# Kernel tuning notes

Measured on AMD Instinct MI355X. Metric: run time of the kernel, lower is better.

## Reference

```python
import jax, jax.numpy as jnp
import numpy as np

IM_SIZE = 32
SCALE = float(IM_SIZE ** 2)  # sqrt(im_size**4)


def setup_inputs() -> dict:
    key = jax.random.key(0)
    kq, kk, kv = jax.random.split(key, 3)
    shape = (2, 8, 64, IM_SIZE, IM_SIZE, 16)  # b n p x y d
    return {
        "query": jax.random.normal(kq, shape, dtype=jnp.float32),
        "key": jax.random.normal(kk, shape, dtype=jnp.float32),
        "value": jax.random.normal(kv, shape, dtype=jnp.float32),
    }


def reference(query, key, value):
    # scores: [b, n, p, q], contraction over the flattened (x, y, d) token field
    scores = jnp.einsum('bnpxyd,bnqxyd->bnpq', query, key) / SCALE
    attention_weights = jax.nn.softmax(scores, axis=-1)
    # dropout p=0.0 (eval mode) -> identity
    out = jnp.einsum('bnpq,bnqxyd->bnpxyd', attention_weights, value)
    out = jnp.transpose(out, (0, 2, 3, 4, 5, 1))  # -> [b, p, x, y, d, n]
    return (out, attention_weights)
```

## Files before the change

### kernel.cpp

```cpp
#include <hip/hip_runtime.h>
#include <hip/hip_bf16.h>

typedef __attribute__((ext_vector_type(8))) short short8;
typedef __attribute__((ext_vector_type(4))) float f32x4;

#define P64 64
#define FDIM 16384
#define OUT0 16777216

__device__ __forceinline__ unsigned short f2bf(float x) {
    unsigned int u = __float_as_uint(x);
    u += 0x7FFFu + ((u >> 16) & 1u);
    return (unsigned short)(u >> 16);
}

__device__ __forceinline__ short8 pack8(float4 v0, float4 v1) {
    short8 r;
    r[0] = (short)f2bf(v0.x); r[1] = (short)f2bf(v0.y);
    r[2] = (short)f2bf(v0.z); r[3] = (short)f2bf(v0.w);
    r[4] = (short)f2bf(v1.x); r[5] = (short)f2bf(v1.y);
    r[6] = (short)f2bf(v1.z); r[7] = (short)f2bf(v1.w);
    return r;
}

__global__ __launch_bounds__(256) void qk_kernel(
        const float* __restrict__ Q, const float* __restrict__ K,
        float* __restrict__ partials) {
    __shared__ float red[4][64 * 65];
    const int bn    = blockIdx.y;
    const int slice = blockIdx.x;
    const int wave  = threadIdx.x >> 6;
    const int lane  = threadIdx.x & 63;
    const int lrow  = lane & 15;
    const int lg    = lane >> 4;
    const int kbase0 = slice * 256 + wave * 64;

    const float* Qb = Q + (size_t)bn * P64 * FDIM;
    const float* Kb = K + (size_t)bn * P64 * FDIM;

    f32x4 acc[4][4];
#pragma unroll
    for (int i = 0; i < 4; i++)
#pragma unroll
        for (int j = 0; j < 4; j++) acc[i][j] = (f32x4){0.f, 0.f, 0.f, 0.f};

#pragma unroll
    for (int ks = 0; ks < 64; ks += 32) {
        const int kb = kbase0 + ks + lg * 8;
        short8 a[4], b[4];
#pragma unroll
        for (int pt = 0; pt < 4; pt++) {
            const float* src = Qb + (size_t)(pt * 16 + lrow) * FDIM + kb;
            a[pt] = pack8(*(const float4*)src, *(const float4*)(src + 4));
        }
#pragma unroll
        for (int qt = 0; qt < 4; qt++) {
            const float* src = Kb + (size_t)(qt * 16 + lrow) * FDIM + kb;
            b[qt] = pack8(*(const float4*)src, *(const float4*)(src + 4));
        }
#pragma unroll
        for (int pt = 0; pt < 4; pt++)
#pragma unroll
            for (int qt = 0; qt < 4; qt++)
                acc[pt][qt] = __builtin_amdgcn_mfma_f32_16x16x32_bf16(
                    a[pt], b[qt], acc[pt][qt], 0, 0, 0);
    }

#pragma unroll
    for (int pt = 0; pt < 4; pt++)
#pragma unroll
        for (int qt = 0; qt < 4; qt++)
#pragma unroll
            for (int r = 0; r < 4; r++) {
                const int p = pt * 16 + lg * 4 + r;
                const int q = qt * 16 + lrow;
                red[wave][p * 65 + q] = acc[pt][qt][r];
            }
    __syncthreads();

    float* dst = partials + ((size_t)bn * 64 + slice) * 4096;
#pragma unroll
    for (int e = threadIdx.x; e < 4096; e += 256) {
        const int p = e >> 6, q = e & 63;
        const int o = p * 65 + q;
        dst[e] = red[0][o] + red[1][o] + red[2][o] + red[3][o];
    }
}

__global__ __launch_bounds__(256) void softmax_kernel(
        const float* __restrict__ partials, float* __restrict__ attn_out) {
    const int wave = threadIdx.x >> 6;
    const int lane = threadIdx.x & 63;
    const int row  = blockIdx.x * 4 + wave;
    const int bn = row >> 6;
    const int p  = row & 63;

    const float* src = partials + (size_t)bn * 64 * 4096 + p * 64 + lane;
    float s = 0.f;
#pragma unroll 8
    for (int sl = 0; sl < 64; sl++) s += src[(size_t)sl * 4096];
    s *= (1.0f / 1024.0f);

    float m = s;
#pragma unroll
    for (int off = 32; off; off >>= 1) m = fmaxf(m, __shfl_xor(m, off, 64));
    const float e = __expf(s - m);
    float sum = e;
#pragma unroll
    for (int off = 32; off; off >>= 1) sum += __shfl_xor(sum, off, 64);
    attn_out[(size_t)row * 64 + lane] = e / sum;
}

__global__ __launch_bounds__(256) void pv_kernel(
        const float* __restrict__ V, const float* __restrict__ attn,
        float* __restrict__ out) {
    const int b  = blockIdx.y;
    const int fc = blockIdx.x * 16;
    const int wave = threadIdx.x >> 6;
    const int lane = threadIdx.x & 63;
    const int pstrip = wave * 16;
    const int lrow = lane & 15;
    const int lg   = lane >> 4;

    f32x4 acc[8];
#pragma unroll
    for (int n = 0; n < 8; n++) acc[n] = (f32x4){0.f, 0.f, 0.f, 0.f};

#pragma unroll
    for (int n = 0; n < 8; n++) {
        const float* An = attn + (size_t)(b * 8 + n) * 64 * 64;
        const float* Vn = V + (size_t)(b * 8 + n) * P64 * FDIM;

#pragma unroll
        for (int kk = 0; kk < 2; kk++) {
            const float* as = An + (size_t)(pstrip + lrow) * 64 + kk * 32 + lg * 8;
            const short8 a = pack8(*(const float4*)as, *(const float4*)(as + 4));
            const float* vs = Vn + (size_t)(kk * 32 + lg * 8) * FDIM + fc + lrow;
            short8 bf;
#pragma unroll
            for (int j = 0; j < 8; j++) bf[j] = (short)f2bf(vs[(size_t)j * FDIM]);
            acc[n] = __builtin_amdgcn_mfma_f32_16x16x32_bf16(a, bf, acc[n], 0, 0, 0);
        }
    }

#pragma unroll
    for (int r = 0; r < 4; r++) {
        const int p = pstrip + lg * 4 + r;
        float4 w0, w1;
        w0.x = acc[0][r]; w0.y = acc[1][r]; w0.z = acc[2][r]; w0.w = acc[3][r];
        w1.x = acc[4][r]; w1.y = acc[5][r]; w1.z = acc[6][r]; w1.w = acc[7][r];
        float* dst = out + ((size_t)(b * 64 + p) * FDIM + fc + lrow) * 8;
        *(float4*)dst       = w0;
        *(float4*)(dst + 4) = w1;
    }
}

extern "C" void kernel_launch(void* const* d_in, const int* in_sizes, int n_in,
                              void* d_out, int out_size, void* d_ws, size_t ws_size,
                              hipStream_t stream) {
    const float* Q = (const float*)d_in[0];
    const float* K = (const float*)d_in[1];
    const float* V = (const float*)d_in[2];
    float* out  = (float*)d_out;
    float* attn = out + OUT0;
    float* partials = (float*)d_ws;

    qk_kernel<<<dim3(64, 16), 256, 0, stream>>>(Q, K, partials);
    softmax_kernel<<<256, 256, 0, stream>>>(partials, attn);
    pv_kernel<<<dim3(1024, 2), 256, 0, stream>>>(V, attn, out);
}
```

Before: 272.5 us.

## Store bf16 per-wave QK partials and stage V tiles in LDS with double-buffering

The QK kernel drops its LDS cross-wave reduction and writes per-wave partial score tiles directly in bf16, so the softmax kernel now reduces 256 slices per row using a block per row. The PV kernel is restructured to load 64-wide V tiles into LDS via global_load_lds with double buffering across heads, so each V element is fetched once per block and coalesced. The aim is to cut strided global V reads and partial-buffer traffic. In exchange, partials are rounded to bf16 before summation, which adds precision loss, and the partials buffer gets larger.

After: 240.4 us. 1.13x faster.

```diff
diff --git a/kernel.cpp b/kernel.cpp
--- a/kernel.cpp
+++ b/kernel.cpp
@@ -4,16 +4,18 @@
 typedef __attribute__((ext_vector_type(8))) short short8;
 typedef __attribute__((ext_vector_type(4))) float f32x4;
 
-#define P64 64
 #define FDIM 16384
 #define OUT0 16777216
+#define NSL  256
 
 __device__ __forceinline__ unsigned short f2bf(float x) {
     unsigned int u = __float_as_uint(x);
     u += 0x7FFFu + ((u >> 16) & 1u);
     return (unsigned short)(u >> 16);
 }
-
+__device__ __forceinline__ float bf2f(unsigned short b) {
+    return __uint_as_float(((unsigned int)b) << 16);
+}
 __device__ __forceinline__ short8 pack8(float4 v0, float4 v1) {
     short8 r;
     r[0] = (short)f2bf(v0.x); r[1] = (short)f2bf(v0.y);
@@ -23,20 +25,18 @@
     return r;
 }
 
-__global__ __launch_bounds__(256) void qk_kernel(
+__global__ __launch_bounds__(256, 4) void qk_kernel(
         const float* __restrict__ Q, const float* __restrict__ K,
-        float* __restrict__ partials) {
-    __shared__ float red[4][64 * 65];
-    const int bn    = blockIdx.y;
-    const int slice = blockIdx.x;
-    const int wave  = threadIdx.x >> 6;
-    const int lane  = threadIdx.x & 63;
-    const int lrow  = lane & 15;
-    const int lg    = lane >> 4;
-    const int kbase0 = slice * 256 + wave * 64;
-
-    const float* Qb = Q + (size_t)bn * P64 * FDIM;
-    const float* Kb = K + (size_t)bn * P64 * FDIM;
+        unsigned short* __restrict__ partials) {
+    const int bn   = blockIdx.y;
+    const int wave = threadIdx.x >> 6;
+    const int lane = threadIdx.x & 63;
+    const int sl   = blockIdx.x * 4 + wave;
+    const int lrow = lane & 15;
+    const int lg   = lane >> 4;
+
+    const float* Qb = Q + (size_t)bn * 64 * FDIM;
+    const float* Kb = K + (size_t)bn * 64 * FDIM;
 
     f32x4 acc[4][4];
 #pragma unroll
@@ -46,7 +46,7 @@
 
 #pragma unroll
     for (int ks = 0; ks < 64; ks += 32) {
-        const int kb = kbase0 + ks + lg * 8;
+        const int kb = sl * 64 + ks + lg * 8;
         short8 a[4], b[4];
 #pragma unroll
         for (int pt = 0; pt < 4; pt++) {
@@ -74,85 +74,143 @@
             for (int r = 0; r < 4; r++) {
                 const int p = pt * 16 + lg * 4 + r;
                 const int q = qt * 16 + lrow;
-                red[wave][p * 65 + q] = acc[pt][qt][r];
+                partials[((size_t)(bn * 64 + p) * NSL + sl) * 64 + q] =
+                    f2bf(acc[pt][qt][r]);
             }
-    __syncthreads();
-
-    float* dst = partials + ((size_t)bn * 64 + slice) * 4096;
-#pragma unroll
-    for (int e = threadIdx.x; e < 4096; e += 256) {
-        const int p = e >> 6, q = e & 63;
-        const int o = p * 65 + q;
-        dst[e] = red[0][o] + red[1][o] + red[2][o] + red[3][o];
-    }
 }
 
 __global__ __launch_bounds__(256) void softmax_kernel(
-        const float* __restrict__ partials, float* __restrict__ attn_out) {
+        const unsigned short* __restrict__ partials, float* __restrict__ attn_out) {
+    __shared__ float red[4][64];
+    const int row  = blockIdx.x;
     const int wave = threadIdx.x >> 6;
     const int lane = threadIdx.x & 63;
-    const int row  = blockIdx.x * 4 + wave;
-    const int bn = row >> 6;
-    const int p  = row & 63;
-
-    const float* src = partials + (size_t)bn * 64 * 4096 + p * 64 + lane;
-    float s = 0.f;
-#pragma unroll 8
-    for (int sl = 0; sl < 64; sl++) s += src[(size_t)sl * 4096];
-    s *= (1.0f / 1024.0f);
-
-    float m = s;
-#pragma unroll
-    for (int off = 32; off; off >>= 1) m = fmaxf(m, __shfl_xor(m, off, 64));
-    const float e = __expf(s - m);
-    float sum = e;
-#pragma unroll
-    for (int off = 32; off; off >>= 1) sum += __shfl_xor(sum, off, 64);
-    attn_out[(size_t)row * 64 + lane] = e / sum;
-}
-
-__global__ __launch_bounds__(256) void pv_kernel(
+    const int gp   = lane >> 3;
+    const int o    = lane & 7;
+    const int g    = wave * 8 + gp;
+
+    const unsigned short* src = partials + (size_t)row * NSL * 64;
+    float s[8] = {0.f, 0.f, 0.f, 0.f, 0.f, 0.f, 0.f, 0.f};
+#pragma unroll
+    for (int i = 0; i < 8; i++) {
+        const int slc = g + 32 * i;
+        const short8 v = *(const short8*)(src + (size_t)slc * 64 + o * 8);
+#pragma unroll
+        for (int j = 0; j < 8; j++) s[j] += bf2f((unsigned short)v[j]);
+    }
+#pragma unroll
+    for (int off = 8; off <= 32; off <<= 1)
+#pragma unroll
+        for (int j = 0; j < 8; j++) s[j] += __shfl_xor(s[j], off, 64);
+    if (lane < 8)
+#pragma unroll
+        for (int j = 0; j < 8; j++) red[wave][lane * 8 + j] = s[j];
+    __syncthreads();
+
+    if (wave == 0) {
+        float t = red[0][lane] + red[1][lane] + red[2][lane] + red[3][lane];
+        t *= (1.0f / 1024.0f);
+        float m = t;
+#pragma unroll
+        for (int off = 32; off; off >>= 1) m = fmaxf(m, __shfl_xor(m, off, 64));
+        const float e = __expf(t - m);
+        float sum = e;
+#pragma unroll
+        for (int off = 32; off; off >>= 1) sum += __shfl_xor(sum, off, 64);
+        attn_out[(size_t)row * 64 + lane] = e / sum;
+    }
+}
+
+__global__ __launch_bounds__(512, 4) void pv_kernel(
         const float* __restrict__ V, const float* __restrict__ attn,
         float* __restrict__ out) {
-    const int b  = blockIdx.y;
-    const int fc = blockIdx.x * 16;
-    const int wave = threadIdx.x >> 6;
+    __shared__ float vt[2][64 * 64];
+    const int b    = blockIdx.y;
+    const int fc   = blockIdx.x * 64;
+    const int w    = threadIdx.x >> 6;
     const int lane = threadIdx.x & 63;
-    const int pstrip = wave * 16;
     const int lrow = lane & 15;
     const int lg   = lane >> 4;
-
-    f32x4 acc[8];
-#pragma unroll
-    for (int n = 0; n < 8; n++) acc[n] = (f32x4){0.f, 0.f, 0.f, 0.f};
-
+    const int pstrip = (w >> 1) * 16;
+    const int fstrip = (w & 1) * 32;
+
+    f32x4 acc[8][2];
+#pragma unroll
+    for (int n = 0; n < 8; n++)
+#pragma unroll
+        for (int ft = 0; ft < 2; ft++) acc[n][ft] = (f32x4){0.f, 0.f, 0.f, 0.f};
+
+#define STAGE(BI, N)                                                          \
+    {                                                                         \
+        const float* Vn_ = V + (size_t)(b * 8 + (N)) * 64 * FDIM;             \
+        _Pragma("unroll")                                                     \
+        for (int c = 0; c < 2; c++) {                                         \
+            const int row_ = w * 8 + c * 4 + lg;                              \
+            const float* src_ = Vn_ + (size_t)row_ * FDIM + fc + lrow * 4;    \
+            __builtin_amdgcn_global_load_lds(                                 \
+                (const __attribute__((address_space(1))) void*)src_,          \
+                (__attribute__((address_space(3))) void*)&vt[BI][row_ * 64 + lrow * 4], \
+                16, 0, 0);                                                    \
+        }                                                                     \
+    }
+
+    STAGE(0, 0);
 #pragma unroll
     for (int n = 0; n < 8; n++) {
-        const float* An = attn + (size_t)(b * 8 + n) * 64 * 64;
-        const float* Vn = V + (size_t)(b * 8 + n) * P64 * FDIM;
-
-#pragma unroll
-        for (int kk = 0; kk < 2; kk++) {
-            const float* as = An + (size_t)(pstrip + lrow) * 64 + kk * 32 + lg * 8;
-            const short8 a = pack8(*(const float4*)as, *(const float4*)(as + 4));
-            const float* vs = Vn + (size_t)(kk * 32 + lg * 8) * FDIM + fc + lrow;
-            short8 bf;
-#pragma unroll
-            for (int j = 0; j < 8; j++) bf[j] = (short)f2bf(vs[(size_t)j * FDIM]);
-            acc[n] = __builtin_amdgcn_mfma_f32_16x16x32_bf16(a, bf, acc[n], 0, 0, 0);
-        }
-    }
-
-#pragma unroll
-    for (int r = 0; r < 4; r++) {
-        const int p = pstrip + lg * 4 + r;
-        float4 w0, w1;
-        w0.x = acc[0][r]; w0.y = acc[1][r]; w0.z = acc[2][r]; w0.w = acc[3][r];
-        w1.x = acc[4][r]; w1.y = acc[5][r]; w1.z = acc[6][r]; w1.w = acc[7][r];
-        float* dst = out + ((size_t)(b * 64 + p) * FDIM + fc + lrow) * 8;
-        *(float4*)dst       = w0;
-        *(float4*)(dst + 4) = w1;
-    }
+        const int cur = n & 1;
+        const float* Ap = attn + (size_t)(b * 8 + n) * 4096 +
+                          (size_t)(pstrip + lrow) * 64 + lg * 8;
+        const float4 a00 = *(const float4*)(Ap);
+        const float4 a01 = *(const float4*)(Ap + 4);
+        const float4 a10 = *(const float4*)(Ap + 32);
+        const float4 a11 = *(const float4*)(Ap + 36);
+
+        if (n < 7) {
+            STAGE(cur ^ 1, n + 1);
+            asm volatile("s_waitcnt vmcnt(2)" ::: "memory");
+        } else {
+            asm volatile("s_waitcnt vmcnt(0)" ::: "memory");
+        }
+        __builtin_amdgcn_s_barrier();
+        __builtin_amdgcn_sched_barrier(0);
+
+        const short8 a0 = pack8(a00, a01);
+        const short8 a1 = pack8(a10, a11);
+
+#pragma unroll
+        for (int ft = 0; ft < 2; ft++) {
+#pragma unroll
+            for (int kk = 0; kk < 2; kk++) {
+                short8 bf;
+#pragma unroll
+                for (int j = 0; j < 8; j++) {
+                    const float vv = vt[cur][(kk * 32 + lg * 8 + j) * 64 +
+                                             fstrip + ft * 16 + lrow];
+                    bf[j] = (short)f2bf(vv);
+                }
+                acc[n][ft] = __builtin_amdgcn_mfma_f32_16x16x32_bf16(
+                    kk ? a1 : a0, bf, acc[n][ft], 0, 0, 0);
+            }
+        }
+        __builtin_amdgcn_s_barrier();
+    }
+
+#pragma unroll
+    for (int ft = 0; ft < 2; ft++)
+#pragma unroll
+        for (int r = 0; r < 4; r++) {
+            const int p = pstrip + lg * 4 + r;
+            const int f = fc + fstrip + ft * 16 + lrow;
+            float4 w0, w1;
+            w0.x = acc[0][ft][r]; w0.y = acc[1][ft][r];
+            w0.z = acc[2][ft][r]; w0.w = acc[3][ft][r];
+            w1.x = acc[4][ft][r]; w1.y = acc[5][ft][r];
+            w1.z = acc[6][ft][r]; w1.w = acc[7][ft][r];
+            float* dst = out + ((size_t)(b * 64 + p) * FDIM + f) * 8;
+            *(float4*)dst       = w0;
+            *(float4*)(dst + 4) = w1;
+        }
+#undef STAGE
 }
 
 extern "C" void kernel_launch(void* const* d_in, const int* in_sizes, int n_in,
@@ -163,9 +221,9 @@
     const float* V = (const float*)d_in[2];
     float* out  = (float*)d_out;
     float* attn = out + OUT0;
-    float* partials = (float*)d_ws;
+    unsigned short* partials = (unsigned short*)d_ws;
 
     qk_kernel<<<dim3(64, 16), 256, 0, stream>>>(Q, K, partials);
-    softmax_kernel<<<256, 256, 0, stream>>>(partials, attn);
-    pv_kernel<<<dim3(1024, 2), 256, 0, stream>>>(V, attn, out);
-}
+    softmax_kernel<<<1024, 256, 0, stream>>>(partials, attn);
+    pv_kernel<<<dim3(256, 2), 512, 0, stream>>>(V, attn, out);
+}
```
